# Optimization experiments

Hardware: AMD Instinct MI355X
Metric: run time of the kernel (lower is better)

The kernel has to match this reference:

```python
import math
import jax, jax.numpy as jnp
import numpy as np

B, H, T, D = 4, 16, 1024, 64


def setup_inputs() -> dict:
    key0 = jax.random.key(0)
    ks = jax.random.split(key0, 5)
    return {
        "query": jax.random.normal(ks[0], (B, H, T, D), dtype=jnp.float32),
        "key": jax.random.normal(ks[1], (B, H, T, D), dtype=jnp.float32),
        "value": jax.random.normal(ks[2], (B, H, T, D), dtype=jnp.float32),
        "edges_key": jax.random.normal(ks[3], (T, T, D), dtype=jnp.float32),
        "edges_value": jax.random.normal(ks[4], (T, T, D), dtype=jnp.float32),
        "mask": jnp.ones((B, 1, 1, T), dtype=bool),
    }


def reference(query, key, value, edges_key, edges_value, mask):
    d = query.shape[-1]
    # content-content scores [B,H,T,T]
    scores = jnp.einsum("bhqd,bhkd->bhqk", query, key)
    # content-position scores via relative edge keys [T,T,D]
    scores = scores + jnp.einsum("bhqd,qkd->bhqk", query, edges_key)
    scores = scores * (1.0 / math.sqrt(d))
    scores = jnp.where(mask, scores, jnp.float32(-1e9))
    a = jax.nn.softmax(scores, axis=-1)  # dropout is identity in eval / pdrop=0
    # value update + relative edge-value update
    out = jnp.einsum("bhqk,bhkd->bhqd", a, value)
    out = out + jnp.einsum("bhqk,qkd->bhqd", a, edges_value)
    return out
```

## Files before the change

kernel.cpp:

```cpp
#include <hip/hip_runtime.h>

#define Tt 1024
#define Dh 64
#define SCALE 0.125f

typedef __attribute__((ext_vector_type(4))) float f32x4;
typedef __attribute__((ext_vector_type(2))) float f32x2;
typedef __attribute__((ext_vector_type(8))) short bf16x8;

__device__ inline unsigned short f2bf(float x){
  __bf16 h = (__bf16)x;
  return __builtin_bit_cast(unsigned short, h);
}
__device__ inline float bf2f(unsigned short h){
  return __uint_as_float(((unsigned)h) << 16);
}
__device__ inline ushort4 pack4(float4 f){
  ushort4 u; u.x=f2bf(f.x); u.y=f2bf(f.y); u.z=f2bf(f.z); u.w=f2bf(f.w); return u;
}
__device__ inline bf16x8 pack8(float4 a, float4 b){
  bf16x8 r;
  r[0]=(short)f2bf(a.x); r[1]=(short)f2bf(a.y); r[2]=(short)f2bf(a.z); r[3]=(short)f2bf(a.w);
  r[4]=(short)f2bf(b.x); r[5]=(short)f2bf(b.y); r[6]=(short)f2bf(b.z); r[7]=(short)f2bf(b.w);
  return r;
}
__device__ inline f32x4 mfma16(bf16x8 a, bf16x8 b, f32x4 c){
  return __builtin_amdgcn_mfma_f32_16x16x32_bf16(a, b, c, 0, 0, 0);
}
__device__ inline unsigned pk8(ushort4 u){
  float f0 = bf2f(u.x)*0.03125f, f1 = bf2f(u.y)*0.03125f;
  float f2_ = bf2f(u.z)*0.03125f, f3 = bf2f(u.w)*0.03125f;
  int r = __builtin_amdgcn_cvt_pk_fp8_f32(f0, f1, 0, false);
  r = __builtin_amdgcn_cvt_pk_fp8_f32(f2_, f3, r, true);
  return (unsigned)r;
}
__device__ inline void up8(unsigned v, float* f){
  f32x2 a = __builtin_amdgcn_cvt_pk_f32_fp8((int)v, false);
  f32x2 b = __builtin_amdgcn_cvt_pk_f32_fp8((int)v, true);
  f[0]=a[0]; f[1]=a[1]; f[2]=b[0]; f[3]=b[1];
}

__device__ inline void stage64x64(const float* __restrict__ g, unsigned short (*lds)[68], int tid){
  int r = tid >> 2, c = (tid & 3) * 16;
  const float4* g4 = (const float4*)(g + (size_t)r * 64 + c);
  float4 f0 = g4[0], f1 = g4[1], f2_ = g4[2], f3 = g4[3];
  ushort4* d4 = (ushort4*)&lds[r][c];
  d4[0]=pack4(f0); d4[1]=pack4(f1); d4[2]=pack4(f2_); d4[3]=pack4(f3);
}
__device__ inline void stage64x64T4(const float* __restrict__ g, unsigned short (*lds)[68], int tid){
  const int kb = (tid >> 4) * 4, db = (tid & 15) * 4;
  float fv[4][4];
#pragma unroll
  for (int j = 0; j < 4; ++j){
    float4 f = *(const float4*)(g + (size_t)(kb + j) * 64 + db);
    fv[j][0]=f.x; fv[j][1]=f.y; fv[j][2]=f.z; fv[j][3]=f.w;
  }
#pragma unroll
  for (int i = 0; i < 4; ++i){
    ushort4 u;
    u.x=f2bf(fv[0][i]); u.y=f2bf(fv[1][i]); u.z=f2bf(fv[2][i]); u.w=f2bf(fv[3][i]);
    *(ushort4*)&lds[db + i][kb] = u;
  }
}
__device__ inline void stage_rows(const unsigned short* __restrict__ g, size_t rowstride,
                                  unsigned short (*lds)[68], int tid){
  int r = tid >> 2, c = (tid & 3) * 16;
  const ushort4* s4 = (const ushort4*)(g + (size_t)r * rowstride + c);
  ushort4 u0=s4[0], u1=s4[1], u2=s4[2], u3=s4[3];
  ushort4* d4 = (ushort4*)&lds[r][c];
  d4[0]=u0; d4[1]=u1; d4[2]=u2; d4[3]=u3;
}
__device__ inline bf16x8 ldsfrag(const unsigned short (*lds)[68], int row, int col){
  const ushort4* p = (const ushort4*)&lds[row][col];
  ushort4 u0 = p[0], u1 = p[1];
  bf16x8 r;
  r[0]=(short)u0.x; r[1]=(short)u0.y; r[2]=(short)u0.z; r[3]=(short)u0.w;
  r[4]=(short)u1.x; r[5]=(short)u1.y; r[6]=(short)u1.z; r[7]=(short)u1.w;
  return r;
}

__global__ __launch_bounds__(256) void k_qek(const float* __restrict__ Q,
                                             const float* __restrict__ EK,
                                             unsigned short* __restrict__ BIAS){
  __shared__ unsigned short ek[2][64][68];
  __shared__ unsigned short ot[4][16][68];
  const int qi = blockIdx.x;
  const int tid = threadIdx.x;
  const int w = tid >> 6, l = tid & 63, lr = l & 15, lg = l >> 4;

  bf16x8 a0, a1;
  {
    const float4* q4 = (const float4*)(Q + ((size_t)(16*w + lr) * Tt + qi) * Dh);
    a0 = pack8(q4[lg*2],     q4[lg*2 + 1]);
    a1 = pack8(q4[8 + lg*2], q4[8 + lg*2 + 1]);
  }
  const float* ekq = EK + (size_t)qi * Tt * Dh;
  const int r = l >> 2, c2 = (l & 3) * 16;
  unsigned short* dst0 = BIAS + (size_t)(16*w + r) * Tt * Tt + (size_t)qi * Tt + c2;

  stage64x64(ekq, ek[0], tid);
  __syncthreads();

  for (int kt = 0; kt < 16; ++kt){
    if (kt < 15) stage64x64(ekq + (size_t)(kt+1) * 64 * Dh, ek[(kt+1)&1], tid);
    const unsigned short (*cur)[68] = ek[kt&1];
    f32x4 acc[4];
#pragma unroll
    for (int c = 0; c < 4; ++c){
      bf16x8 b0 = ldsfrag(cur, c*16 + lr, lg*8);
      bf16x8 b1 = ldsfrag(cur, c*16 + lr, lg*8 + 32);
      f32x4 z = {0.f,0.f,0.f,0.f};
      z = mfma16(a0, b0, z);
      z = mfma16(a1, b1, z);
      acc[c] = z;
    }
#pragma unroll
    for (int c = 0; c < 4; ++c)
#pragma unroll
      for (int j = 0; j < 4; ++j)
        ot[w][lg*4 + j][c*16 + lr] = f2bf(acc[c][j]);
    __builtin_amdgcn_wave_barrier();
    {
      const ushort4* s4 = (const ushort4*)&ot[w][r][c2];
      ushort4 u0=s4[0], u1=s4[1], u2=s4[2], u3=s4[3];
      ushort4* d4 = (ushort4*)(dst0 + kt*64);
      d4[0]=u0; d4[1]=u1; d4[2]=u2; d4[3]=u3;
    }
    __builtin_amdgcn_wave_barrier();
    __syncthreads();
  }
}

__global__ __launch_bounds__(256) void k_attn(const float* __restrict__ Q,
                                              const float* __restrict__ K,
                                              const float* __restrict__ V,
                                              const unsigned short* __restrict__ BIAS,
                                              unsigned char* __restrict__ P8,
                                              float* __restrict__ OUT){
  __shared__ unsigned short kt_[64][68];
  __shared__ unsigned short bt[64][68];
  __shared__ unsigned short pt[64][68];
  __shared__ unsigned short vt[64][68];
  const int bid = blockIdx.x;
  const int bh = (bid & 7) + ((bid >> 7) << 3);
  const int qt = ((bid >> 3) & 15) * 64;
  const int tid = threadIdx.x;
  const int w = tid >> 6, l = tid & 63, lr = l & 15, lg = l >> 4;

  bf16x8 a0, a1;
  {
    const float4* q4 = (const float4*)(Q + ((size_t)bh * Tt + qt + 16*w + lr) * Dh);
    a0 = pack8(q4[lg*2],     q4[lg*2 + 1]);
    a1 = pack8(q4[8 + lg*2], q4[8 + lg*2 + 1]);
  }
  const float* kb = K + (size_t)bh * Tt * Dh;
  const float* vb = V + (size_t)bh * Tt * Dh;
  const unsigned short* bsb = BIAS + (size_t)bh * Tt * Tt;
  unsigned char* p8b = P8 + (size_t)bh * Tt * Tt;

  float lsum[4] = {0.f,0.f,0.f,0.f};
  f32x4 oacc[4];
#pragma unroll
  for (int c = 0; c < 4; ++c) oacc[c] = (f32x4){0.f,0.f,0.f,0.f};

  for (int kt = 0; kt < 16; ++kt){
    stage64x64(kb + (size_t)kt * 64 * Dh, kt_, tid);
    stage_rows(bsb + (size_t)qt * Tt + kt*64, Tt, bt, tid);
    stage64x64T4(vb + (size_t)kt * 64 * Dh, vt, tid);
    __syncthreads();
#pragma unroll
    for (int c = 0; c < 4; ++c){
      bf16x8 b0 = ldsfrag(kt_, c*16 + lr, lg*8);
      bf16x8 b1 = ldsfrag(kt_, c*16 + lr, lg*8 + 32);
      f32x4 z = {0.f,0.f,0.f,0.f};
      z = mfma16(a0, b0, z);
      z = mfma16(a1, b1, z);
      int kl = c*16 + lr;
#pragma unroll
      for (int j = 0; j < 4; ++j){
        float s = (z[j] + bf2f(bt[16*w + lg*4 + j][kl])) * SCALE;
        float p = __expf(s);
        lsum[j] += p;
        pt[16*w + lg*4 + j][kl] = f2bf(p);
      }
    }
    __builtin_amdgcn_wave_barrier();
    bf16x8 p0 = ldsfrag(pt, 16*w + lr, lg*8);
    bf16x8 p1 = ldsfrag(pt, 16*w + lr, lg*8 + 32);
#pragma unroll
    for (int c = 0; c < 4; ++c){
      bf16x8 v0 = ldsfrag(vt, c*16 + lr, lg*8);
      bf16x8 v1 = ldsfrag(vt, c*16 + lr, lg*8 + 32);
      oacc[c] = mfma16(p0, v0, oacc[c]);
      oacc[c] = mfma16(p1, v1, oacc[c]);
    }
    {
      int r = l >> 2, cq = (l & 3);
      const ushort4* s4 = (const ushort4*)&pt[16*w + r][cq*16];
      ushort4 u0=s4[0], u1=s4[1], u2=s4[2], u3=s4[3];
      uint4 o;
      o.x = pk8(u0); o.y = pk8(u1); o.z = pk8(u2); o.w = pk8(u3);
      *(uint4*)(p8b + ((size_t)(qt + 16*w + r) << 10) + kt*64 + cq*16) = o;
    }
    __syncthreads();
  }
  float rl[4];
#pragma unroll
  for (int j = 0; j < 4; ++j){
    float su = lsum[j];
    for (int o = 1; o < 16; o <<= 1) su += __shfl_xor(su, o, 64);
    rl[j] = 1.f / su;
  }
#pragma unroll
  for (int c = 0; c < 4; ++c)
#pragma unroll
    for (int j = 0; j < 4; ++j)
      OUT[((size_t)bh * Tt + qt + 16*w + lg*4 + j) * Dh + c*16 + lr] = oacc[c][j] * rl[j];
}

__global__ __launch_bounds__(256) void k_aev(const unsigned char* __restrict__ P8,
                                             const float* __restrict__ EV,
                                             float* __restrict__ OUT){
  __shared__ unsigned short evt[2][64][68];
  __shared__ float sums[64];
  const int qi = blockIdx.x;
  const int tid = threadIdx.x;
  const int w = tid >> 6, l = tid & 63, lr = l & 15, lg = l >> 4;

  const unsigned char* arow = P8 + (size_t)(16*w + lr) * Tt * Tt + (size_t)qi * Tt;
  const float* evq = EV + (size_t)qi * Tt * Dh;

  f32x4 acc[4];
#pragma unroll
  for (int c = 0; c < 4; ++c) acc[c] = (f32x4){0.f,0.f,0.f,0.f};
  float asum = 0.f;

  stage64x64T4(evq, evt[0], tid);
  __syncthreads();

  for (int kt = 0; kt < 16; ++kt){
    if (kt < 15) stage64x64T4(evq + (size_t)(kt+1) * 64 * Dh, evt[(kt+1)&1], tid);
    const unsigned short (*cur)[68] = evt[kt&1];
    uint2 ua = *(const uint2*)(arow + kt*64 + lg*8);
    uint2 ub = *(const uint2*)(arow + kt*64 + 32 + lg*8);
    float fa[8], fb[8];
    up8(ua.x, fa); up8(ua.y, fa+4);
    up8(ub.x, fb); up8(ub.y, fb+4);
    bf16x8 a0, a1;
#pragma unroll
    for (int i = 0; i < 8; ++i){
      asum += fa[i] + fb[i];
      a0[i] = (short)f2bf(fa[i]);
      a1[i] = (short)f2bf(fb[i]);
    }
#pragma unroll
    for (int c = 0; c < 4; ++c){
      bf16x8 b0 = ldsfrag(cur, c*16 + lr, lg*8);
      bf16x8 b1 = ldsfrag(cur, c*16 + lr, lg*8 + 32);
      acc[c] = mfma16(a0, b0, acc[c]);
      acc[c] = mfma16(a1, b1, acc[c]);
    }
    __syncthreads();
  }
  asum += __shfl_xor(asum, 16, 64);
  asum += __shfl_xor(asum, 32, 64);
  if (lg == 0) sums[16*w + lr] = asum;
  __builtin_amdgcn_wave_barrier();

#pragma unroll
  for (int c = 0; c < 4; ++c)
#pragma unroll
    for (int j = 0; j < 4; ++j){
      int bh = 16*w + lg*4 + j;
      float rl = 1.f / sums[bh];
      size_t idx = ((size_t)bh * Tt + qi) * Dh + c*16 + lr;
      OUT[idx] += acc[c][j] * rl;
    }
}

extern "C" void kernel_launch(void* const* d_in, const int* in_sizes, int n_in,
                              void* d_out, int out_size, void* d_ws, size_t ws_size,
                              hipStream_t stream){
  const float* Q  = (const float*)d_in[0];
  const float* K  = (const float*)d_in[1];
  const float* V  = (const float*)d_in[2];
  const float* EK = (const float*)d_in[3];
  const float* EV = (const float*)d_in[4];
  float* OUT = (float*)d_out;
  unsigned short* BIAS = (unsigned short*)d_ws;
  unsigned char*  P8   = (unsigned char*)(BIAS + (size_t)64*Tt*Tt);

  if (ws_size < (size_t)64*Tt*Tt*sizeof(unsigned short) + (size_t)64*Tt*Tt) return;

  k_qek <<<dim3(1024), dim3(256), 0, stream>>>(Q, EK, BIAS);
  k_attn<<<dim3(1024), dim3(256), 0, stream>>>(Q, K, V, BIAS, P8, OUT);
  k_aev <<<dim3(1024), dim3(256), 0, stream>>>(P8, EV, OUT);
}
```

Baseline: 255.5 us.

## Swap MFMA operand roles so waves split keys, keep P in registers

Both k_qek and k_attn now assign each wave a 16-key slice and compute transposed score tiles (key as A operand, query as B) across all 64 query rows. In k_attn the probabilities stay in registers and feed a 16x16x16 bf16 MFMA directly, which removes the P round-trip through LDS and its intra-wave barrier, and the fp8 P is written straight from registers. Because each wave now holds partial output for every query, the four waves' accumulators are reduced serially through an LDS scratch buffer at the end. k_qek drops its double buffering and its LDS transpose, writing bias directly as 4-element chunks. The cost is much larger register pressure (16 output accumulators), narrower 8-byte and 4-byte global stores, and extra barriers in the epilogue.

```diff
diff --git a/kernel.cpp b/kernel.cpp
--- a/kernel.cpp
+++ b/kernel.cpp
@@ -7,6 +7,7 @@
 typedef __attribute__((ext_vector_type(4))) float f32x4;
 typedef __attribute__((ext_vector_type(2))) float f32x2;
 typedef __attribute__((ext_vector_type(8))) short bf16x8;
+typedef __attribute__((ext_vector_type(4))) short bf16x4;
 
 __device__ inline unsigned short f2bf(float x){
   __bf16 h = (__bf16)x;
@@ -27,11 +28,18 @@
 __device__ inline f32x4 mfma16(bf16x8 a, bf16x8 b, f32x4 c){
   return __builtin_amdgcn_mfma_f32_16x16x32_bf16(a, b, c, 0, 0, 0);
 }
-__device__ inline unsigned pk8(ushort4 u){
-  float f0 = bf2f(u.x)*0.03125f, f1 = bf2f(u.y)*0.03125f;
-  float f2_ = bf2f(u.z)*0.03125f, f3 = bf2f(u.w)*0.03125f;
-  int r = __builtin_amdgcn_cvt_pk_fp8_f32(f0, f1, 0, false);
-  r = __builtin_amdgcn_cvt_pk_fp8_f32(f2_, f3, r, true);
+__device__ inline f32x4 mfma16k16(bf16x4 a, bf16x4 b, f32x4 c){
+#if __has_builtin(__builtin_amdgcn_mfma_f32_16x16x16bf16_1k)
+  return __builtin_amdgcn_mfma_f32_16x16x16bf16_1k(a, b, c, 0, 0, 0);
+#else
+  asm volatile("v_mfma_f32_16x16x16_bf16 %0, %1, %2, %0\n\ts_nop 7\n\ts_nop 7"
+               : "+v"(c) : "v"(a), "v"(b));
+  return c;
+#endif
+}
+__device__ inline unsigned pk8f(const float* p){
+  int r = __builtin_amdgcn_cvt_pk_fp8_f32(p[0]*0.03125f, p[1]*0.03125f, 0, false);
+  r = __builtin_amdgcn_cvt_pk_fp8_f32(p[2]*0.03125f, p[3]*0.03125f, r, true);
   return (unsigned)r;
 }
 __device__ inline void up8(unsigned v, float* f){
@@ -82,51 +90,35 @@
 __global__ __launch_bounds__(256) void k_qek(const float* __restrict__ Q,
                                              const float* __restrict__ EK,
                                              unsigned short* __restrict__ BIAS){
-  __shared__ unsigned short ek[2][64][68];
-  __shared__ unsigned short ot[4][16][68];
+  __shared__ unsigned short ek[64][68];
   const int qi = blockIdx.x;
   const int tid = threadIdx.x;
   const int w = tid >> 6, l = tid & 63, lr = l & 15, lg = l >> 4;
 
-  bf16x8 a0, a1;
-  {
-    const float4* q4 = (const float4*)(Q + ((size_t)(16*w + lr) * Tt + qi) * Dh);
-    a0 = pack8(q4[lg*2],     q4[lg*2 + 1]);
-    a1 = pack8(q4[8 + lg*2], q4[8 + lg*2 + 1]);
+  bf16x8 qf[4][2];
+#pragma unroll
+  for (int bq = 0; bq < 4; ++bq){
+    const float4* q4 = (const float4*)(Q + ((size_t)(bq*16 + lr) * Tt + qi) * Dh);
+    qf[bq][0] = pack8(q4[lg*2],     q4[lg*2 + 1]);
+    qf[bq][1] = pack8(q4[8 + lg*2], q4[8 + lg*2 + 1]);
   }
   const float* ekq = EK + (size_t)qi * Tt * Dh;
-  const int r = l >> 2, c2 = (l & 3) * 16;
-  unsigned short* dst0 = BIAS + (size_t)(16*w + r) * Tt * Tt + (size_t)qi * Tt + c2;
-
-  stage64x64(ekq, ek[0], tid);
-  __syncthreads();
 
   for (int kt = 0; kt < 16; ++kt){
-    if (kt < 15) stage64x64(ekq + (size_t)(kt+1) * 64 * Dh, ek[(kt+1)&1], tid);
-    const unsigned short (*cur)[68] = ek[kt&1];
-    f32x4 acc[4];
-#pragma unroll
-    for (int c = 0; c < 4; ++c){
-      bf16x8 b0 = ldsfrag(cur, c*16 + lr, lg*8);
-      bf16x8 b1 = ldsfrag(cur, c*16 + lr, lg*8 + 32);
+    stage64x64(ekq + (size_t)kt * 64 * Dh, ek, tid);
+    __syncthreads();
+    bf16x8 ea0 = ldsfrag(ek, w*16 + lr, lg*8);
+    bf16x8 ea1 = ldsfrag(ek, w*16 + lr, lg*8 + 32);
+#pragma unroll
+    for (int bq = 0; bq < 4; ++bq){
       f32x4 z = {0.f,0.f,0.f,0.f};
-      z = mfma16(a0, b0, z);
-      z = mfma16(a1, b1, z);
-      acc[c] = z;
-    }
-#pragma unroll
-    for (int c = 0; c < 4; ++c)
-#pragma unroll
-      for (int j = 0; j < 4; ++j)
-        ot[w][lg*4 + j][c*16 + lr] = f2bf(acc[c][j]);
-    __builtin_amdgcn_wave_barrier();
-    {
-      const ushort4* s4 = (const ushort4*)&ot[w][r][c2];
-      ushort4 u0=s4[0], u1=s4[1], u2=s4[2], u3=s4[3];
-      ushort4* d4 = (ushort4*)(dst0 + kt*64);
-      d4[0]=u0; d4[1]=u1; d4[2]=u2; d4[3]=u3;
-    }
-    __builtin_amdgcn_wave_barrier();
+      z = mfma16(ea0, qf[bq][0], z);
+      z = mfma16(ea1, qf[bq][1], z);
+      ushort4 u;
+      u.x=f2bf(z[0]); u.y=f2bf(z[1]); u.z=f2bf(z[2]); u.w=f2bf(z[3]);
+      *(ushort4*)(BIAS + (size_t)(bq*16 + lr) * Tt * Tt + (size_t)qi * Tt
+                  + kt*64 + w*16 + lg*4) = u;
+    }
     __syncthreads();
   }
 }
@@ -139,19 +131,22 @@
                                               float* __restrict__ OUT){
   __shared__ unsigned short kt_[64][68];
   __shared__ unsigned short bt[64][68];
-  __shared__ unsigned short pt[64][68];
   __shared__ unsigned short vt[64][68];
+  __shared__ float wsum[4][64];
+  __shared__ float sums[64];
+  __shared__ float scratch[64][68];
   const int bid = blockIdx.x;
   const int bh = (bid & 7) + ((bid >> 7) << 3);
   const int qt = ((bid >> 3) & 15) * 64;
   const int tid = threadIdx.x;
   const int w = tid >> 6, l = tid & 63, lr = l & 15, lg = l >> 4;
 
-  bf16x8 a0, a1;
-  {
-    const float4* q4 = (const float4*)(Q + ((size_t)bh * Tt + qt + 16*w + lr) * Dh);
-    a0 = pack8(q4[lg*2],     q4[lg*2 + 1]);
-    a1 = pack8(q4[8 + lg*2], q4[8 + lg*2 + 1]);
+  bf16x8 qf[4][2];
+#pragma unroll
+  for (int qq = 0; qq < 4; ++qq){
+    const float4* q4 = (const float4*)(Q + ((size_t)bh * Tt + qt + qq*16 + lr) * Dh);
+    qf[qq][0] = pack8(q4[lg*2],     q4[lg*2 + 1]);
+    qf[qq][1] = pack8(q4[8 + lg*2], q4[8 + lg*2 + 1]);
   }
   const float* kb = K + (size_t)bh * Tt * Dh;
   const float* vb = V + (size_t)bh * Tt * Dh;
@@ -159,63 +154,82 @@
   unsigned char* p8b = P8 + (size_t)bh * Tt * Tt;
 
   float lsum[4] = {0.f,0.f,0.f,0.f};
-  f32x4 oacc[4];
-#pragma unroll
-  for (int c = 0; c < 4; ++c) oacc[c] = (f32x4){0.f,0.f,0.f,0.f};
+  f32x4 oacc[4][4];
+#pragma unroll
+  for (int a = 0; a < 4; ++a)
+#pragma unroll
+    for (int b = 0; b < 4; ++b) oacc[a][b] = (f32x4){0.f,0.f,0.f,0.f};
 
   for (int kt = 0; kt < 16; ++kt){
     stage64x64(kb + (size_t)kt * 64 * Dh, kt_, tid);
     stage_rows(bsb + (size_t)qt * Tt + kt*64, Tt, bt, tid);
     stage64x64T4(vb + (size_t)kt * 64 * Dh, vt, tid);
     __syncthreads();
-#pragma unroll
-    for (int c = 0; c < 4; ++c){
-      bf16x8 b0 = ldsfrag(kt_, c*16 + lr, lg*8);
-      bf16x8 b1 = ldsfrag(kt_, c*16 + lr, lg*8 + 32);
+    bf16x8 ka0 = ldsfrag(kt_, w*16 + lr, lg*8);
+    bf16x8 ka1 = ldsfrag(kt_, w*16 + lr, lg*8 + 32);
+    bf16x4 vf[4];
+#pragma unroll
+    for (int dq = 0; dq < 4; ++dq)
+      vf[dq] = *(const bf16x4*)&vt[dq*16 + lr][w*16 + lg*4];
+#pragma unroll
+    for (int qq = 0; qq < 4; ++qq){
       f32x4 z = {0.f,0.f,0.f,0.f};
-      z = mfma16(a0, b0, z);
-      z = mfma16(a1, b1, z);
-      int kl = c*16 + lr;
-#pragma unroll
-      for (int j = 0; j < 4; ++j){
-        float s = (z[j] + bf2f(bt[16*w + lg*4 + j][kl])) * SCALE;
-        float p = __expf(s);
-        lsum[j] += p;
-        pt[16*w + lg*4 + j][kl] = f2bf(p);
-      }
-    }
-    __builtin_amdgcn_wave_barrier();
-    bf16x8 p0 = ldsfrag(pt, 16*w + lr, lg*8);
-    bf16x8 p1 = ldsfrag(pt, 16*w + lr, lg*8 + 32);
-#pragma unroll
-    for (int c = 0; c < 4; ++c){
-      bf16x8 v0 = ldsfrag(vt, c*16 + lr, lg*8);
-      bf16x8 v1 = ldsfrag(vt, c*16 + lr, lg*8 + 32);
-      oacc[c] = mfma16(p0, v0, oacc[c]);
-      oacc[c] = mfma16(p1, v1, oacc[c]);
-    }
-    {
-      int r = l >> 2, cq = (l & 3);
-      const ushort4* s4 = (const ushort4*)&pt[16*w + r][cq*16];
-      ushort4 u0=s4[0], u1=s4[1], u2=s4[2], u3=s4[3];
-      uint4 o;
-      o.x = pk8(u0); o.y = pk8(u1); o.z = pk8(u2); o.w = pk8(u3);
-      *(uint4*)(p8b + ((size_t)(qt + 16*w + r) << 10) + kt*64 + cq*16) = o;
-    }
-    __syncthreads();
-  }
-  float rl[4];
-#pragma unroll
-  for (int j = 0; j < 4; ++j){
-    float su = lsum[j];
-    for (int o = 1; o < 16; o <<= 1) su += __shfl_xor(su, o, 64);
-    rl[j] = 1.f / su;
-  }
-#pragma unroll
-  for (int c = 0; c < 4; ++c)
-#pragma unroll
-    for (int j = 0; j < 4; ++j)
-      OUT[((size_t)bh * Tt + qt + 16*w + lg*4 + j) * Dh + c*16 + lr] = oacc[c][j] * rl[j];
+      z = mfma16(ka0, qf[qq][0], z);
+      z = mfma16(ka1, qf[qq][1], z);
+      ushort4 bv = *(const ushort4*)&bt[qq*16 + lr][w*16 + lg*4];
+      float p[4];
+      p[0] = __expf((z[0] + bf2f(bv.x)) * SCALE);
+      p[1] = __expf((z[1] + bf2f(bv.y)) * SCALE);
+      p[2] = __expf((z[2] + bf2f(bv.z)) * SCALE);
+      p[3] = __expf((z[3] + bf2f(bv.w)) * SCALE);
+      lsum[qq] += p[0] + p[1] + p[2] + p[3];
+      *(unsigned*)(p8b + (size_t)(qt + qq*16 + lr) * Tt + kt*64 + w*16 + lg*4) = pk8f(p);
+      bf16x4 pf;
+      pf[0]=(short)f2bf(p[0]); pf[1]=(short)f2bf(p[1]);
+      pf[2]=(short)f2bf(p[2]); pf[3]=(short)f2bf(p[3]);
+#pragma unroll
+      for (int dq = 0; dq < 4; ++dq)
+        oacc[qq][dq] = mfma16k16(pf, vf[dq], oacc[qq][dq]);
+    }
+    __syncthreads();
+  }
+#pragma unroll
+  for (int qq = 0; qq < 4; ++qq){
+    float su = lsum[qq];
+    su += __shfl_xor(su, 16, 64);
+    su += __shfl_xor(su, 32, 64);
+    if (lg == 0) wsum[w][qq*16 + lr] = su;
+  }
+  __syncthreads();
+  if (tid < 64) sums[tid] = wsum[0][tid] + wsum[1][tid] + wsum[2][tid] + wsum[3][tid];
+#pragma unroll
+  for (int ww = 0; ww < 4; ++ww){
+    __syncthreads();
+    if (w == ww){
+#pragma unroll
+      for (int qq = 0; qq < 4; ++qq)
+#pragma unroll
+        for (int dq = 0; dq < 4; ++dq)
+#pragma unroll
+          for (int j = 0; j < 4; ++j){
+            float* s = &scratch[qq*16 + lg*4 + j][dq*16 + lr];
+            if (ww == 0) *s = oacc[qq][dq][j];
+            else         *s += oacc[qq][dq][j];
+          }
+    }
+  }
+  __syncthreads();
+  {
+    int r = tid >> 2, c4 = (tid & 3) * 16;
+    float rlv = 1.f / sums[r];
+    float* op = OUT + ((size_t)bh * Tt + qt + r) * Dh + c4;
+#pragma unroll
+    for (int i = 0; i < 4; ++i){
+      float4 v = *(const float4*)&scratch[r][c4 + i*4];
+      v.x *= rlv; v.y *= rlv; v.z *= rlv; v.w *= rlv;
+      *(float4*)(op + i*4) = v;
+    }
+  }
 }
 
 __global__ __launch_bounds__(256) void k_aev(const unsigned char* __restrict__ P8,
```

After: 323.0 us. 26.4% more time.
